# Performance work log

Hardware: AMD Instinct MI355X
Metric: run time of the kernel (lower is better)

## Reference

```python
import jax, jax.numpy as jnp
import numpy as np

B, T, V, L = 131072, 6, 31, 3  # batch, seq_len, vocab/hidden, num RNN layers


def setup_inputs() -> dict:
    key = jax.random.key(0)
    ks = jax.random.split(key, 8)
    s = 1.0 / np.sqrt(V)  # torch default init scale for RNN/Linear
    return {
        "inp": jax.random.normal(ks[0], (B, T, V), dtype=jnp.float32),
        "h0": jax.random.normal(ks[1], (L, B, V), dtype=jnp.float32),
        "W_ih": jax.random.uniform(ks[2], (L, V, V), jnp.float32, -s, s),
        "W_hh": jax.random.uniform(ks[3], (L, V, V), jnp.float32, -s, s),
        "b_ih": jax.random.uniform(ks[4], (L, V), jnp.float32, -s, s),
        "b_hh": jax.random.uniform(ks[5], (L, V), jnp.float32, -s, s),
        "W_lin": jax.random.uniform(ks[6], (V, V), jnp.float32, -s, s),
        "b_lin": jax.random.uniform(ks[7], (V,), jnp.float32, -s, s),
    }


def _rnn_layer(x_tm, h0_l, wih, whh, bih, bhh):
    # x_tm: [T, B, V] time-major; h0_l: [B, V]
    def step(h, x_t):
        h_new = jnp.tanh(x_t @ wih.T + bih + h @ whh.T + bhh)
        return h_new, h_new

    _, ys = jax.lax.scan(step, h0_l, x_tm)
    return ys  # [T, B, V]


def reference(inp, h0, W_ih, W_hh, b_ih, b_hh, W_lin, b_lin):
    x = jnp.transpose(inp, (1, 0, 2))  # [T, B, V] time-major
    for l in range(L):
        x = _rnn_layer(x, h0[l], W_ih[l], W_hh[l], b_ih[l], b_hh[l])
    y = jnp.tanh(x @ W_lin.T + b_lin)  # [T, B, V]
    last = y[-1]  # [B, V] == y[:, -1, :] in batch-major
    return jax.nn.softmax(last, axis=1)
```

## Files before the change

kernel.cpp:

```cpp
#include <hip/hip_runtime.h>
#include <hip/hip_bf16.h>


#define VD 31
#define TD 6
#define LROW 40
#define LBUF (16 * LROW)

typedef __attribute__((ext_vector_type(8))) short bf16x8;
typedef __attribute__((ext_vector_type(4))) float f32x4;
typedef __attribute__((ext_vector_type(4))) unsigned u32x4;
typedef float f32x4u __attribute__((ext_vector_type(4), aligned(4)));

struct raw8 { f32x4u a, b; };

__device__ __forceinline__ short f2bf(float f) {
    unsigned u = __float_as_uint(f);
    unsigned r = (u + 0x7fffu + ((u >> 16) & 1u)) >> 16;
    return (short)r;
}

__device__ __forceinline__ unsigned f2bf2u(float lo, float hi) {
    union { __hip_bfloat162 h2; unsigned u; } cvt;
    cvt.h2 = __float22bfloat162_rn(make_float2(lo, hi));
    return cvt.u;
}

__device__ __forceinline__ float fast_tanh(float x) {
    x = fminf(fmaxf(x, -15.0f), 15.0f);
    float e = __expf(2.0f * x);
    return (e - 1.0f) * __builtin_amdgcn_rcpf(e + 1.0f);
}

__device__ __forceinline__ raw8 load_raw(const float* __restrict__ p, int fo) {
    raw8 r;
    r.a = *(const f32x4u*)(p + fo);
    r.b = *(const f32x4u*)(p + fo + 4);
    return r;
}

__device__ __forceinline__ bf16x8 cvt_frag(raw8 r, bool q3) {
    float l[8] = {r.a[0], r.a[1], r.a[2], r.a[3], r.b[0], r.b[1], r.b[2], r.b[3]};
    float s[8];
#pragma unroll
    for (int j = 0; j < 7; ++j) s[j] = q3 ? l[j + 1] : l[j];
    s[7] = q3 ? 0.0f : l[7];
    union { u32x4 u4; bf16x8 b8; } cvt;
#pragma unroll
    for (int j = 0; j < 4; ++j) cvt.u4[j] = f2bf2u(s[2 * j], s[2 * j + 1]);
    return cvt.b8;
}

__device__ __forceinline__ bf16x8 load_wfrag(const float* __restrict__ W,
                                             int nn, int k0) {
    bf16x8 r;
#pragma unroll
    for (int j = 0; j < 8; ++j) {
        int k = k0 + j;
        float v = (nn < VD && k < VD) ? W[nn * VD + k] : 0.0f;
        r[j] = f2bf(v);
    }
    return r;
}

__device__ __forceinline__ bf16x8 layer_step(
    bf16x8 ax, bf16x8 ah,
    bf16x8 wi0, bf16x8 wi1, bf16x8 wh0, bf16x8 wh1,
    float b0, float b1, short* buf, int n, int quad, int k0)
{
    f32x4 c0 = {b0, b0, b0, b0};
    f32x4 c1 = {b1, b1, b1, b1};
    c0 = __builtin_amdgcn_mfma_f32_16x16x32_bf16(ax, wi0, c0, 0, 0, 0);
    c1 = __builtin_amdgcn_mfma_f32_16x16x32_bf16(ax, wi1, c1, 0, 0, 0);
    c0 = __builtin_amdgcn_mfma_f32_16x16x32_bf16(ah, wh0, c0, 0, 0, 0);
    c1 = __builtin_amdgcn_mfma_f32_16x16x32_bf16(ah, wh1, c1, 0, 0, 0);
#pragma unroll
    for (int r = 0; r < 4; ++r) {
        int row = quad * 4 + r;
        unsigned u = f2bf2u(fast_tanh(c0[r]), fast_tanh(c1[r]));
        buf[row * LROW + n]      = (short)u;
        buf[row * LROW + 16 + n] = (short)(u >> 16);
    }
    __builtin_amdgcn_wave_barrier();
    return *(const bf16x8*)(buf + n * LROW + k0);
}

__global__ __launch_bounds__(256, 1) void rnn_mfma(
    const float* __restrict__ inp,
    const float* __restrict__ h0,
    const float* __restrict__ Wih,
    const float* __restrict__ Whh,
    const float* __restrict__ bih,
    const float* __restrict__ bhh,
    const float* __restrict__ Wlin,
    const float* __restrict__ blin,
    float* __restrict__ out,
    int B)
{
    __shared__ __align__(16) short lds[4][2][2][LBUF];

    const int wave = threadIdx.x >> 6;
    const int lane = threadIdx.x & 63;
    const int n    = lane & 15;
    const int quad = lane >> 4;
    const int k0   = quad * 8;
    const bool q3  = (quad == 3);
    const int fo   = q3 ? 23 : k0;
    const int bbase = (blockIdx.x * 4 + wave) * 32;
    if (bbase >= B) return;

    const float* W0 = Wih;               const float* U0 = Whh;
    const float* W1 = Wih + VD * VD;     const float* U1 = Whh + VD * VD;
    const float* W2 = Wih + 2 * VD * VD; const float* U2 = Whh + 2 * VD * VD;
    const bf16x8 wiA0 = load_wfrag(W0, n, k0),   wiA1 = load_wfrag(W0, n + 16, k0);
    const bf16x8 whA0 = load_wfrag(U0, n, k0),   whA1 = load_wfrag(U0, n + 16, k0);
    const bf16x8 wiB0 = load_wfrag(W1, n, k0),   wiB1 = load_wfrag(W1, n + 16, k0);
    const bf16x8 whB0 = load_wfrag(U1, n, k0),   whB1 = load_wfrag(U1, n + 16, k0);
    const bf16x8 wiC0 = load_wfrag(W2, n, k0),   wiC1 = load_wfrag(W2, n + 16, k0);
    const bf16x8 whC0 = load_wfrag(U2, n, k0),   whC1 = load_wfrag(U2, n + 16, k0);
    const bf16x8 wl0  = load_wfrag(Wlin, n, k0), wl1  = load_wfrag(Wlin, n + 16, k0);

    const bool hi_ok = (n + 16) < VD;
    const float bsA0 = bih[n] + bhh[n];
    const float bsA1 = hi_ok ? bih[n + 16] + bhh[n + 16] : 0.0f;
    const float bsB0 = bih[VD + n] + bhh[VD + n];
    const float bsB1 = hi_ok ? bih[VD + n + 16] + bhh[VD + n + 16] : 0.0f;
    const float bsC0 = bih[2 * VD + n] + bhh[2 * VD + n];
    const float bsC1 = hi_ok ? bih[2 * VD + n + 16] + bhh[2 * VD + n + 16] : 0.0f;
    const float bl0  = blin[n];
    const float bl1  = hi_ok ? blin[n + 16] : 0.0f;

    bf16x8 a1a = cvt_frag(load_raw(h0 + ((size_t)0 * B + bbase + n) * VD, fo), q3);
    bf16x8 a1b = cvt_frag(load_raw(h0 + ((size_t)0 * B + bbase + 16 + n) * VD, fo), q3);
    bf16x8 a2a = cvt_frag(load_raw(h0 + ((size_t)1 * B + bbase + n) * VD, fo), q3);
    bf16x8 a2b = cvt_frag(load_raw(h0 + ((size_t)1 * B + bbase + 16 + n) * VD, fo), q3);
    bf16x8 a3a = cvt_frag(load_raw(h0 + ((size_t)2 * B + bbase + n) * VD, fo), q3);
    bf16x8 a3b = cvt_frag(load_raw(h0 + ((size_t)2 * B + bbase + 16 + n) * VD, fo), q3);

    const float* xrow0 = inp + (size_t)(bbase + n) * TD * VD;
    const float* xrow1 = inp + (size_t)(bbase + 16 + n) * TD * VD;

    raw8 rx0 = load_raw(xrow0, fo);
    raw8 rx1 = load_raw(xrow1, fo);

    int p = 0;
    for (int t = 0; t < TD; ++t) {
        bf16x8 ax0 = cvt_frag(rx0, q3);
        bf16x8 ax1 = cvt_frag(rx1, q3);
        if (t + 1 < TD) {
            rx0 = load_raw(xrow0 + (t + 1) * VD, fo);
            rx1 = load_raw(xrow1 + (t + 1) * VD, fo);
        }
        a1a = layer_step(ax0, a1a, wiA0, wiA1, whA0, whA1, bsA0, bsA1,
                         lds[wave][0][p], n, quad, k0);
        a1b = layer_step(ax1, a1b, wiA0, wiA1, whA0, whA1, bsA0, bsA1,
                         lds[wave][1][p], n, quad, k0);
        p ^= 1;
        a2a = layer_step(a1a, a2a, wiB0, wiB1, whB0, whB1, bsB0, bsB1,
                         lds[wave][0][p], n, quad, k0);
        a2b = layer_step(a1b, a2b, wiB0, wiB1, whB0, whB1, bsB0, bsB1,
                         lds[wave][1][p], n, quad, k0);
        p ^= 1;
        a3a = layer_step(a2a, a3a, wiC0, wiC1, whC0, whC1, bsC0, bsC1,
                         lds[wave][0][p], n, quad, k0);
        a3b = layer_step(a2b, a3b, wiC0, wiC1, whC0, whC1, bsC0, bsC1,
                         lds[wave][1][p], n, quad, k0);
        p ^= 1;
    }

    f32x4 c0a = {bl0, bl0, bl0, bl0}, c1a = {bl1, bl1, bl1, bl1};
    f32x4 c0b = {bl0, bl0, bl0, bl0}, c1b = {bl1, bl1, bl1, bl1};
    c0a = __builtin_amdgcn_mfma_f32_16x16x32_bf16(a3a, wl0, c0a, 0, 0, 0);
    c1a = __builtin_amdgcn_mfma_f32_16x16x32_bf16(a3a, wl1, c1a, 0, 0, 0);
    c0b = __builtin_amdgcn_mfma_f32_16x16x32_bf16(a3b, wl0, c0b, 0, 0, 0);
    c1b = __builtin_amdgcn_mfma_f32_16x16x32_bf16(a3b, wl1, c1b, 0, 0, 0);

    const bool pad = (n == 15);
#pragma unroll
    for (int r = 0; r < 4; ++r) {
#pragma unroll
        for (int tb = 0; tb < 2; ++tb) {
            float v0 = fast_tanh(tb ? c0b[r] : c0a[r]);
            float v1 = fast_tanh(tb ? c1b[r] : c1a[r]);
            float mx = pad ? v0 : fmaxf(v0, v1);
#pragma unroll
            for (int msk = 1; msk < 16; msk <<= 1)
                mx = fmaxf(mx, __shfl_xor(mx, msk, 16));
            float e0 = __expf(v0 - mx);
            float e1 = pad ? 0.0f : __expf(v1 - mx);
            float s = e0 + e1;
#pragma unroll
            for (int msk = 1; msk < 16; msk <<= 1)
                s += __shfl_xor(s, msk, 16);
            float inv = __builtin_amdgcn_rcpf(s);
            const size_t row = (size_t)(bbase + tb * 16 + quad * 4 + r);
            out[row * VD + n] = e0 * inv;
            if (!pad) out[row * VD + 16 + n] = e1 * inv;
        }
    }
}

extern "C" void kernel_launch(void* const* d_in, const int* in_sizes, int n_in,
                              void* d_out, int out_size, void* d_ws, size_t ws_size,
                              hipStream_t stream) {
    const float* inp  = (const float*)d_in[0];
    const float* h0   = (const float*)d_in[1];
    const float* Wih  = (const float*)d_in[2];
    const float* Whh  = (const float*)d_in[3];
    const float* bih  = (const float*)d_in[4];
    const float* bhh  = (const float*)d_in[5];
    const float* Wlin = (const float*)d_in[6];
    const float* blin = (const float*)d_in[7];
    float* out = (float*)d_out;

    const int B = in_sizes[0] / (TD * VD);
    const int grid = (B + 127) / 128;
    rnn_mfma<<<grid, 256, 0, stream>>>(inp, h0, Wih, Whh, bih, bhh, Wlin, blin, out, B);
}
```

Baseline: 217.2 us.

## Process four 16-row batch tiles per wave and simplify tanh

Each wave now handles four 16-row tiles instead of two, which halves the grid and interleaves more independent MFMA and tanh chains per layer step to hide latency. The explicit wave barrier is replaced by a compiler signal fence between the LDS write and read. tanh drops its clamp and becomes 1 - 2/(e+1). The larger per-wave tile raises register and LDS use and leaves fewer waves to spread across the CUs, so occupancy and load balance may suffer.

```diff
diff --git a/kernel.cpp b/kernel.cpp
--- a/kernel.cpp
+++ b/kernel.cpp
@@ -4,6 +4,7 @@
 
 #define VD 31
 #define TD 6
+#define NT 4
 #define LROW 40
 #define LBUF (16 * LROW)
 
@@ -27,9 +28,8 @@
 }
 
 __device__ __forceinline__ float fast_tanh(float x) {
-    x = fminf(fmaxf(x, -15.0f), 15.0f);
     float e = __expf(2.0f * x);
-    return (e - 1.0f) * __builtin_amdgcn_rcpf(e + 1.0f);
+    return fmaf(-2.0f, __builtin_amdgcn_rcpf(e + 1.0f), 1.0f);
 }
 
 __device__ __forceinline__ raw8 load_raw(const float* __restrict__ p, int fo) {
@@ -63,10 +63,10 @@
     return r;
 }
 
-__device__ __forceinline__ bf16x8 layer_step(
+__device__ __forceinline__ void step_compute(
     bf16x8 ax, bf16x8 ah,
     bf16x8 wi0, bf16x8 wi1, bf16x8 wh0, bf16x8 wh1,
-    float b0, float b1, short* buf, int n, int quad, int k0)
+    float b0, float b1, short* buf, int n, int quad)
 {
     f32x4 c0 = {b0, b0, b0, b0};
     f32x4 c1 = {b1, b1, b1, b1};
@@ -76,12 +76,14 @@
     c1 = __builtin_amdgcn_mfma_f32_16x16x32_bf16(ah, wh1, c1, 0, 0, 0);
 #pragma unroll
     for (int r = 0; r < 4; ++r) {
+        unsigned u = f2bf2u(fast_tanh(c0[r]), fast_tanh(c1[r]));
         int row = quad * 4 + r;
-        unsigned u = f2bf2u(fast_tanh(c0[r]), fast_tanh(c1[r]));
         buf[row * LROW + n]      = (short)u;
         buf[row * LROW + 16 + n] = (short)(u >> 16);
     }
-    __builtin_amdgcn_wave_barrier();
+}
+
+__device__ __forceinline__ bf16x8 step_read(const short* buf, int n, int k0) {
     return *(const bf16x8*)(buf + n * LROW + k0);
 }
 
@@ -97,7 +99,7 @@
     float* __restrict__ out,
     int B)
 {
-    __shared__ __align__(16) short lds[4][2][2][LBUF];
+    __shared__ __align__(16) short lds[4][NT][2][LBUF];
 
     const int wave = threadIdx.x >> 6;
     const int lane = threadIdx.x & 63;
@@ -106,7 +108,7 @@
     const int k0   = quad * 8;
     const bool q3  = (quad == 3);
     const int fo   = q3 ? 23 : k0;
-    const int bbase = (blockIdx.x * 4 + wave) * 32;
+    const int bbase = (blockIdx.x * 4 + wave) * (NT * 16);
     if (bbase >= B) return;
 
     const float* W0 = Wih;               const float* U0 = Whh;
@@ -130,58 +132,66 @@
     const float bl0  = blin[n];
     const float bl1  = hi_ok ? blin[n + 16] : 0.0f;
 
-    bf16x8 a1a = cvt_frag(load_raw(h0 + ((size_t)0 * B + bbase + n) * VD, fo), q3);
-    bf16x8 a1b = cvt_frag(load_raw(h0 + ((size_t)0 * B + bbase + 16 + n) * VD, fo), q3);
-    bf16x8 a2a = cvt_frag(load_raw(h0 + ((size_t)1 * B + bbase + n) * VD, fo), q3);
-    bf16x8 a2b = cvt_frag(load_raw(h0 + ((size_t)1 * B + bbase + 16 + n) * VD, fo), q3);
-    bf16x8 a3a = cvt_frag(load_raw(h0 + ((size_t)2 * B + bbase + n) * VD, fo), q3);
-    bf16x8 a3b = cvt_frag(load_raw(h0 + ((size_t)2 * B + bbase + 16 + n) * VD, fo), q3);
-
-    const float* xrow0 = inp + (size_t)(bbase + n) * TD * VD;
-    const float* xrow1 = inp + (size_t)(bbase + 16 + n) * TD * VD;
-
-    raw8 rx0 = load_raw(xrow0, fo);
-    raw8 rx1 = load_raw(xrow1, fo);
+    bf16x8 a1[NT], a2[NT], a3[NT];
+    raw8 rx[NT];
+    const float* xrow[NT];
+#pragma unroll
+    for (int i = 0; i < NT; ++i) {
+        const int row = bbase + i * 16 + n;
+        a1[i] = cvt_frag(load_raw(h0 + ((size_t)0 * B + row) * VD, fo), q3);
+        a2[i] = cvt_frag(load_raw(h0 + ((size_t)1 * B + row) * VD, fo), q3);
+        a3[i] = cvt_frag(load_raw(h0 + ((size_t)2 * B + row) * VD, fo), q3);
+        xrow[i] = inp + (size_t)row * TD * VD;
+        rx[i] = load_raw(xrow[i], fo);
+    }
 
     int p = 0;
+#pragma unroll 1
     for (int t = 0; t < TD; ++t) {
-        bf16x8 ax0 = cvt_frag(rx0, q3);
-        bf16x8 ax1 = cvt_frag(rx1, q3);
+        bf16x8 ax[NT];
+#pragma unroll
+        for (int i = 0; i < NT; ++i) ax[i] = cvt_frag(rx[i], q3);
         if (t + 1 < TD) {
-            rx0 = load_raw(xrow0 + (t + 1) * VD, fo);
-            rx1 = load_raw(xrow1 + (t + 1) * VD, fo);
-        }
-        a1a = layer_step(ax0, a1a, wiA0, wiA1, whA0, whA1, bsA0, bsA1,
-                         lds[wave][0][p], n, quad, k0);
-        a1b = layer_step(ax1, a1b, wiA0, wiA1, whA0, whA1, bsA0, bsA1,
-                         lds[wave][1][p], n, quad, k0);
+#pragma unroll
+            for (int i = 0; i < NT; ++i) rx[i] = load_raw(xrow[i] + (t + 1) * VD, fo);
+        }
+#pragma unroll
+        for (int i = 0; i < NT; ++i) {
+            step_compute(ax[i], a1[i], wiA0, wiA1, whA0, whA1, bsA0, bsA1,
+                         lds[wave][i][p], n, quad);
+            __atomic_signal_fence(__ATOMIC_SEQ_CST);
+            a1[i] = step_read(lds[wave][i][p], n, k0);
+        }
         p ^= 1;
-        a2a = layer_step(a1a, a2a, wiB0, wiB1, whB0, whB1, bsB0, bsB1,
-                         lds[wave][0][p], n, quad, k0);
-        a2b = layer_step(a1b, a2b, wiB0, wiB1, whB0, whB1, bsB0, bsB1,
-                         lds[wave][1][p], n, quad, k0);
+#pragma unroll
+        for (int i = 0; i < NT; ++i) {
+            step_compute(a1[i], a2[i], wiB0, wiB1, whB0, whB1, bsB0, bsB1,
+                         lds[wave][i][p], n, quad);
+            __atomic_signal_fence(__ATOMIC_SEQ_CST);
+            a2[i] = step_read(lds[wave][i][p], n, k0);
+        }
         p ^= 1;
-        a3a = layer_step(a2a, a3a, wiC0, wiC1, whC0, whC1, bsC0, bsC1,
-                         lds[wave][0][p], n, quad, k0);
-        a3b = layer_step(a2b, a3b, wiC0, wiC1, whC0, whC1, bsC0, bsC1,
-                         lds[wave][1][p], n, quad, k0);
+#pragma unroll
+        for (int i = 0; i < NT; ++i) {
+            step_compute(a2[i], a3[i], wiC0, wiC1, whC0, whC1, bsC0, bsC1,
+                         lds[wave][i][p], n, quad);
+            __atomic_signal_fence(__ATOMIC_SEQ_CST);
+            a3[i] = step_read(lds[wave][i][p], n, k0);
+        }
         p ^= 1;
     }
 
-    f32x4 c0a = {bl0, bl0, bl0, bl0}, c1a = {bl1, bl1, bl1, bl1};
-    f32x4 c0b = {bl0, bl0, bl0, bl0}, c1b = {bl1, bl1, bl1, bl1};
-    c0a = __builtin_amdgcn_mfma_f32_16x16x32_bf16(a3a, wl0, c0a, 0, 0, 0);
-    c1a = __builtin_amdgcn_mfma_f32_16x16x32_bf16(a3a, wl1, c1a, 0, 0, 0);
-    c0b = __builtin_amdgcn_mfma_f32_16x16x32_bf16(a3b, wl0, c0b, 0, 0, 0);
-    c1b = __builtin_amdgcn_mfma_f32_16x16x32_bf16(a3b, wl1, c1b, 0, 0, 0);
-
     const bool pad = (n == 15);
 #pragma unroll
-    for (int r = 0; r < 4; ++r) {
-#pragma unroll
-        for (int tb = 0; tb < 2; ++tb) {
-            float v0 = fast_tanh(tb ? c0b[r] : c0a[r]);
-            float v1 = fast_tanh(tb ? c1b[r] : c1a[r]);
+    for (int i = 0; i < NT; ++i) {
+        f32x4 c0 = {bl0, bl0, bl0, bl0};
+        f32x4 c1 = {bl1, bl1, bl1, bl1};
+        c0 = __builtin_amdgcn_mfma_f32_16x16x32_bf16(a3[i], wl0, c0, 0, 0, 0);
+        c1 = __builtin_amdgcn_mfma_f32_16x16x32_bf16(a3[i], wl1, c1, 0, 0, 0);
+#pragma unroll
+        for (int r = 0; r < 4; ++r) {
+            float v0 = fast_tanh(c0[r]);
+            float v1 = fast_tanh(c1[r]);
             float mx = pad ? v0 : fmaxf(v0, v1);
 #pragma unroll
             for (int msk = 1; msk < 16; msk <<= 1)
@@ -193,7 +203,7 @@
             for (int msk = 1; msk < 16; msk <<= 1)
                 s += __shfl_xor(s, msk, 16);
             float inv = __builtin_amdgcn_rcpf(s);
-            const size_t row = (size_t)(bbase + tb * 16 + quad * 4 + r);
+            const size_t row = (size_t)(bbase + i * 16 + quad * 4 + r);
             out[row * VD + n] = e0 * inv;
             if (!pad) out[row * VD + 16 + n] = e1 * inv;
         }
@@ -214,6 +224,7 @@
     float* out = (float*)d_out;
 
     const int B = in_sizes[0] / (TD * VD);
-    const int grid = (B + 127) / 128;
+    const int rows_per_block = 4 * NT * 16;
+    const int grid = (B + rows_per_block - 1) / rows_per_block;
     rnn_mfma<<<grid, 256, 0, stream>>>(inp, h0, Wih, Whh, bih, bhh, Wlin, blin, out, B);
 }
```

After: 223.0 us. +2.7%, slower.
